# Kernel optimization log

Hardware: AMD Instinct MI355X
Metric: run time of the kernel (lower is better)

## Reference

```python
import jax, jax.numpy as jnp
import numpy as np

N = 50000; E = 800000; B = 500; L = 42
F_IN = 35; HEADS = 10; F_H = 35; F_G = 350
VOCAB = 26; EMB = 128; NF = 16; OUT_DIM = 128; K = 8
NEG_SLOPE = 0.2


def setup_inputs() -> dict:
    key = jax.random.key(0)
    ks = jax.random.split(key, 16)
    inp = {}
    inp['x'] = jax.random.normal(ks[0], (N, F_IN), jnp.float32)
    inp['edge_index'] = jax.random.randint(ks[1], (2, E), 0, N, dtype=jnp.int32)
    inp['batch'] = jnp.sort(jax.random.randint(ks[2], (N,), 0, B, dtype=jnp.int32))
    inp['target'] = jax.random.randint(ks[3], (B, L), 0, VOCAB, dtype=jnp.int32)
    # --- learned parameters ---
    inp['W_gat'] = jax.random.normal(ks[4], (F_IN, HEADS * F_H), jnp.float32) * 0.1
    inp['att_src'] = jax.random.normal(ks[5], (HEADS, F_H), jnp.float32) * 0.1
    inp['att_dst'] = jax.random.normal(ks[6], (HEADS, F_H), jnp.float32) * 0.1
    inp['b_gat'] = jnp.zeros((HEADS * F_H,), jnp.float32)
    inp['W_gcn'] = jax.random.normal(ks[7], (F_G, F_G), jnp.float32) * 0.05
    inp['b_gcn'] = jnp.zeros((F_G,), jnp.float32)
    inp['W_fcg1'] = jax.random.normal(ks[8], (2 * F_G, 1500), jnp.float32) * 0.03
    inp['b_fcg1'] = jnp.zeros((1500,), jnp.float32)
    inp['W_fcg2'] = jax.random.normal(ks[9], (1500, OUT_DIM), jnp.float32) * 0.03
    inp['b_fcg2'] = jnp.zeros((OUT_DIM,), jnp.float32)
    inp['emb_xt'] = jax.random.normal(ks[10], (VOCAB, EMB), jnp.float32) * 0.1
    inp['W_conv'] = jax.random.normal(ks[11], (NF, EMB, K), jnp.float32) * 0.05
    inp['b_conv'] = jnp.zeros((NF,), jnp.float32)
    inp['W_fcxt'] = jax.random.normal(ks[12], (NF * 35, OUT_DIM), jnp.float32) * 0.05
    inp['b_fcxt'] = jnp.zeros((OUT_DIM,), jnp.float32)
    inp['W_fc1'] = jax.random.normal(ks[13], (256, 512), jnp.float32) * 0.05
    inp['b_fc1'] = jnp.zeros((512,), jnp.float32)
    inp['W_out'] = jax.random.normal(ks[14], (512, 1), jnp.float32) * 0.05
    inp['b_out'] = jnp.zeros((1,), jnp.float32)
    return inp


def _add_self_loops(edge_index):
    loop = jnp.arange(N, dtype=edge_index.dtype)
    src = jnp.concatenate([edge_index[0], loop])
    dst = jnp.concatenate([edge_index[1], loop])
    return src, dst


def _gat_conv(x, src, dst, W, att_src, att_dst, b):
    # h: [N, H, C]
    h = (x @ W).reshape(N, HEADS, F_H)
    a_s = jnp.einsum('nhc,hc->nh', h, att_src)  # [N, H]
    a_d = jnp.einsum('nhc,hc->nh', h, att_dst)
    e = jax.nn.leaky_relu(a_s[src] + a_d[dst], NEG_SLOPE)  # [Etot, H]
    # segment softmax over incoming edges per destination node, per head
    m = jax.ops.segment_max(e, dst, num_segments=N)
    m = jnp.where(jnp.isfinite(m), m, 0.0)
    ex = jnp.exp(e - m[dst])
    den = jax.ops.segment_sum(ex, dst, num_segments=N)
    alpha = ex / (den[dst] + 1e-16)  # [Etot, H]
    out = jax.ops.segment_sum(h[src] * alpha[:, :, None], dst, num_segments=N)
    return out.reshape(N, HEADS * F_H) + b, alpha


def _gcn_conv(x, src, dst, W, b):
    deg = jax.ops.segment_sum(jnp.ones_like(dst, jnp.float32), dst, num_segments=N)
    dinv = jnp.where(deg > 0, deg ** -0.5, 0.0)
    norm = dinv[src] * dinv[dst]  # symmetric normalization
    h = x @ W
    return jax.ops.segment_sum(h[src] * norm[:, None], dst, num_segments=N) + b


def reference(x, edge_index, batch, target, W_gat, att_src, att_dst, b_gat,
              W_gcn, b_gcn, W_fcg1, b_fcg1, W_fcg2, b_fcg2, emb_xt,
              W_conv, b_conv, W_fcxt, b_fcxt, W_fc1, b_fc1, W_out, b_out):
    src, dst = _add_self_loops(edge_index)
    # --- graph branch ---
    xg, alpha = _gat_conv(x, src, dst, W_gat, att_src, att_dst, b_gat)
    xg = jax.nn.relu(xg)
    xg = jax.nn.relu(_gcn_conv(xg, src, dst, W_gcn, b_gcn))
    # global max + mean pool per graph
    gmax = jax.ops.segment_max(xg, batch, num_segments=B)
    gsum = jax.ops.segment_sum(xg, batch, num_segments=B)
    cnt = jax.ops.segment_sum(jnp.ones((N,), jnp.float32), batch, num_segments=B)
    gmean = gsum / jnp.maximum(cnt, 1.0)[:, None]
    xg = jnp.concatenate([gmax, gmean], axis=1)  # [B, 700]
    xg = jax.nn.relu(xg @ W_fcg1 + b_fcg1)
    xg = xg @ W_fcg2 + b_fcg2  # [B, 128] (dropout is identity in eval)
    # --- protein branch ---
    emb = emb_xt[target]                      # [B, L, 128]
    emb = jnp.transpose(emb, (0, 2, 1))       # [B, 128, L]
    conv = jax.lax.conv_general_dilated(
        emb, W_conv, window_strides=(1,), padding='VALID',
        dimension_numbers=('NCH', 'OIH', 'NCH'))  # [B, 16, 35]
    conv = conv + b_conv[None, :, None]
    xt = conv.reshape(B, NF * 35)
    xt = xt @ W_fcxt + b_fcxt                 # [B, 128]
    # --- fusion ---
    xc = jnp.concatenate([xg, xt], axis=1)    # [B, 256]
    xc = jax.nn.relu(xc @ W_fc1 + b_fc1)
    out = jax.nn.sigmoid(xc @ W_out + b_out)  # [B, 1]
    return out, alpha
```

## Files before the change

kernel.cpp:

```cpp
#include <hip/hip_runtime.h>
#include <math.h>

#define NN 50000
#define EE 800000
#define BB 500
#define LL 42
#define NHEAD 10
#define FH 35
#define FG 350
#define ETOT (EE + NN)
#define NCHUNK ((NN + 511) / 512)

#define KPAD 384
#define MPAD 50048
#define MB2  512

typedef unsigned short ushort_t;
typedef __attribute__((ext_vector_type(8))) short short8v;
typedef __attribute__((ext_vector_type(4))) float float4v;

__device__ __forceinline__ float lrelu(float x) { return x > 0.f ? x : 0.2f * x; }

__device__ __forceinline__ ushort_t f2bf(float f) {
    unsigned int u = __float_as_uint(f);
    u += 0x7fffu + ((u >> 16) & 1u);
    return (ushort_t)(u >> 16);
}
__device__ __forceinline__ float bflo(unsigned u) { return __uint_as_float(u << 16); }
__device__ __forceinline__ float bfhi(unsigned u) { return __uint_as_float(u & 0xffff0000u); }
__device__ __forceinline__ float bfu(ushort_t u) { return __uint_as_float(((unsigned)u) << 16); }

__device__ __forceinline__ void async_cp16(const void* g, void* l) {
    __builtin_amdgcn_global_load_lds((const __attribute__((address_space(1))) unsigned int*)g,
                                     (__attribute__((address_space(3))) unsigned int*)l, 16, 0, 0);
}

__global__ __launch_bounds__(256) void k_init(int* deg, int* cur) {
    int i = blockIdx.x * 256 + threadIdx.x;
    if (i < NN) { deg[i] = 1; cur[i] = 0; }
}

__global__ __launch_bounds__(256) void k_deg(const int* __restrict__ ei, int* deg) {
    int i = blockIdx.x * 256 + threadIdx.x;
    if (i < EE) atomicAdd(&deg[ei[EE + i]], 1);
}

__global__ __launch_bounds__(512) void k_scan1(const int* __restrict__ deg, int* part) {
    int i = blockIdx.x * 512 + threadIdx.x;
    int lane = threadIdx.x & 63, wv = threadIdx.x >> 6;
    int x = (i < NN) ? deg[i] : 0;
    #pragma unroll
    for (int d = 32; d; d >>= 1) x += __shfl_xor(x, d);
    __shared__ int wsum[8];
    if (lane == 0) wsum[wv] = x;
    __syncthreads();
    if (threadIdx.x == 0) {
        int s = 0;
        #pragma unroll
        for (int w = 0; w < 8; w++) s += wsum[w];
        part[blockIdx.x] = s;
    }
}

__global__ __launch_bounds__(64) void k_scan2(const int* __restrict__ part, int* pscan) {
    int l = threadIdx.x;
    int v0 = (l < NCHUNK) ? part[l] : 0;
    #pragma unroll
    for (int d = 1; d < 64; d <<= 1) { int t = __shfl_up(v0, d); if (l >= d) v0 += t; }
    int tot0 = __shfl(v0, 63);
    int v1 = (64 + l < NCHUNK) ? part[64 + l] : 0;
    #pragma unroll
    for (int d = 1; d < 64; d <<= 1) { int t = __shfl_up(v1, d); if (l >= d) v1 += t; }
    v1 += tot0;
    if (l < NCHUNK) pscan[l] = v0;
    if (64 + l < NCHUNK) pscan[64 + l] = v1;
}

__global__ __launch_bounds__(512) void k_scan3(const int* __restrict__ deg, const int* __restrict__ pscan,
                                               int* offs) {
    int i = blockIdx.x * 512 + threadIdx.x;
    int lane = threadIdx.x & 63, wv = threadIdx.x >> 6;
    int x = (i < NN) ? deg[i] : 0;
    int incl = x;
    #pragma unroll
    for (int d = 1; d < 64; d <<= 1) { int t = __shfl_up(incl, d); if (lane >= d) incl += t; }
    __shared__ int wtot[8];
    if (lane == 63) wtot[wv] = incl;
    __syncthreads();
    int woff = 0;
    for (int w = 0; w < wv; w++) woff += wtot[w];
    int base = (blockIdx.x == 0) ? 0 : pscan[blockIdx.x - 1];
    if (i < NN) offs[i] = base + woff + incl - x;
}

__global__ __launch_bounds__(256) void k_scatter(const int* __restrict__ ei, const int* __restrict__ offs,
                                                 int* cur, int* csr_src) {
    int i = blockIdx.x * 256 + threadIdx.x;
    if (i < EE) {
        int s = ei[i], d = ei[EE + i];
        int slot = atomicAdd(&cur[d], 1);
        csr_src[offs[d] + slot] = s;
    } else if (i < ETOT) {
        int v = i - EE;
        int slot = atomicAdd(&cur[v], 1);
        csr_src[offs[v] + slot] = v;
    }
}

__global__ __launch_bounds__(256) void k_dinv(const int* __restrict__ deg, float* dinv) {
    int i = blockIdx.x * 256 + threadIdx.x;
    if (i < NN) dinv[i] = rsqrtf((float)deg[i]);
}

__global__ __launch_bounds__(256) void k_prep_xf(const float* __restrict__ x, ushort_t* __restrict__ xfb) {
    int i = blockIdx.x * 256 + threadIdx.x;
    if (i >= NN * 40) return;
    int n = i / 40, c = i % 40;
    xfb[i] = (c < 35) ? f2bf(x[n * 35 + c]) : (ushort_t)0;
}

__global__ __launch_bounds__(256) void k_prep_att(const float* __restrict__ W_gat, const float* __restrict__ att_s,
                                                  const float* __restrict__ att_d,
                                                  float* __restrict__ wS, float* __restrict__ wD) {
    int i = blockIdx.x * 256 + threadIdx.x;
    if (i >= FG) return;
    int hd = i / 35, c = i % 35;
    float ss = 0.f, dd = 0.f;
    for (int cc = 0; cc < 35; cc++) {
        float w = W_gat[c * FG + hd * 35 + cc];
        ss += w * att_s[hd * 35 + cc];
        dd += w * att_d[hd * 35 + cc];
    }
    wS[i] = ss;
    wD[i] = dd;
}

__global__ __launch_bounds__(256) void k_prep_wbd(const float* __restrict__ W_gat, ushort_t* __restrict__ Wt) {
    int i = blockIdx.x * 256 + threadIdx.x;
    if (i >= KPAD * KPAD) return;
    int n = i / KPAD, k = i % KPAD;
    float v = 0.f;
    if (n < FG && k < FG && (k / 35) == (n / 35)) v = W_gat[(k % 35) * FG + n];
    Wt[i] = f2bf(v);
}

__global__ __launch_bounds__(256) void k_prep_wgcn(const float* __restrict__ W, ushort_t* __restrict__ Wt) {
    int i = blockIdx.x * 256 + threadIdx.x;
    if (i >= KPAD * KPAD) return;
    int n = i / KPAD, k = i % KPAD;
    float v = (n < FG && k < FG) ? W[k * FG + n] : 0.f;
    Wt[i] = f2bf(v);
}

__global__ __launch_bounds__(256) void k_prep_w(const float* __restrict__ W, ushort_t* __restrict__ Wt,
                                                int K, int N, int KP, int NP) {
    int i = blockIdx.x * 256 + threadIdx.x;
    if (i >= KP * NP) return;
    int k = i / NP, n = i % NP;
    float v = (k < K && n < N) ? W[(size_t)k * N + n] : 0.f;
    Wt[(size_t)n * KP + k] = f2bf(v);
}

__global__ __launch_bounds__(256) void k_cast_pad(const float* __restrict__ src, ushort_t* __restrict__ dst,
                                                  int M, int K, int MP, int KP) {
    int i = blockIdx.x * 256 + threadIdx.x;
    if (i >= MP * KP) return;
    int r = i / KP, k = i % KP;
    dst[i] = (r < M && k < K) ? f2bf(src[(size_t)r * K + k]) : (ushort_t)0;
}

__global__ __launch_bounds__(256) void k_mfma(const ushort_t* __restrict__ A, const ushort_t* __restrict__ Bt,
                                              void* __restrict__ C, int M, int Nv, int ldc, int lda,
                                              int ksteps, const float* __restrict__ bias, int act, int bf16out,
                                              int bdiag) {
    __shared__ ushort_t As[128 * 64];
    __shared__ ushort_t Bs[64 * 64];
    int tid = threadIdx.x;
    int wid = tid >> 6, lane = tid & 63;
    int m0 = blockIdx.y * 128, n0 = blockIdx.x * 64;
    int wm0 = (wid >> 1) * 64, wn0 = (wid & 1) * 32;
    int srow = tid >> 3;
    int scol = (tid & 7) * 8;
    float4v acc[4][2] = {{{0.f,0.f,0.f,0.f},{0.f,0.f,0.f,0.f}},
                         {{0.f,0.f,0.f,0.f},{0.f,0.f,0.f,0.f}},
                         {{0.f,0.f,0.f,0.f},{0.f,0.f,0.f,0.f}},
                         {{0.f,0.f,0.f,0.f},{0.f,0.f,0.f,0.f}}};
    int a_off = (wm0 + (lane & 15)) * 64 + (lane >> 4) * 8;
    int b_off = (wn0 + (lane & 15)) * 64 + (lane >> 4) * 8;
    int ks0 = 0, ks1 = ksteps;
    if (bdiag) {
        int hlo = n0 / 35;
        int hhi = (n0 + 63) / 35; if (hhi > 9) hhi = 9;
        ks0 = (hlo * 35) >> 6;
        ks1 = ((hhi + 1) * 35 + 63) >> 6;
    }
    for (int ks = ks0; ks < ks1; ks++) {
        int k0 = ks * 64;
        #pragma unroll
        for (int r = 0; r < 4; r++) {
            const ushort_t* g = A + (size_t)(m0 + r * 32 + srow) * lda + k0 + scol;
            async_cp16(g, As + (r * 256 + tid) * 8);
        }
        #pragma unroll
        for (int r = 0; r < 2; r++) {
            const ushort_t* g = Bt + (size_t)(n0 + r * 32 + srow) * lda + k0 + scol;
            async_cp16(g, Bs + (r * 256 + tid) * 8);
        }
        __syncthreads();
        #pragma unroll
        for (int kh = 0; kh < 2; kh++) {
            short8v b0 = *(const short8v*)&Bs[b_off + kh * 32];
            short8v b1 = *(const short8v*)&Bs[b_off + 16 * 64 + kh * 32];
            #pragma unroll
            for (int mi = 0; mi < 4; mi++) {
                short8v a = *(const short8v*)&As[a_off + mi * 16 * 64 + kh * 32];
                acc[mi][0] = __builtin_amdgcn_mfma_f32_16x16x32_bf16(a, b0, acc[mi][0], 0, 0, 0);
                acc[mi][1] = __builtin_amdgcn_mfma_f32_16x16x32_bf16(a, b1, acc[mi][1], 0, 0, 0);
            }
        }
        __syncthreads();
    }
    int lm = m0 + wm0 + (lane >> 4) * 4;
    int lc = n0 + wn0 + (lane & 15);
    #pragma unroll
    for (int mi = 0; mi < 4; mi++) {
        #pragma unroll
        for (int ni = 0; ni < 2; ni++) {
            int col = lc + ni * 16;
            float bv = (bias != nullptr && col < Nv) ? bias[col] : 0.f;
            #pragma unroll
            for (int r = 0; r < 4; r++) {
                int row = lm + mi * 16 + r;
                if (row >= M) continue;
                float v = acc[mi][ni][r] + bv;
                if (act) v = fmaxf(v, 0.f);
                if (col >= Nv) v = 0.f;
                if (bf16out) ((ushort_t*)C)[(size_t)row * ldc + col] = f2bf(v);
                else         ((float*)C)[(size_t)row * ldc + col] = v;
            }
        }
    }
}

__global__ __launch_bounds__(256) void k_att2(const float* __restrict__ x, const float* __restrict__ wS,
                                              const float* __restrict__ wD, float* __restrict__ a_s,
                                              float* __restrict__ a_d) {
    int tid = blockIdx.x * 256 + threadIdx.x;
    if (tid >= NN * NHEAD) return;
    int n = tid / NHEAD, hd = tid % NHEAD;
    const float* xr = x + (size_t)n * 35;
    const float* ws = wS + hd * 35;
    const float* wd = wD + hd * 35;
    float as = 0.f, ad = 0.f;
    #pragma unroll
    for (int c = 0; c < 35; c++) { float v = xr[c]; as += v * ws[c]; ad += v * wd[c]; }
    a_s[tid] = as;
    a_d[tid] = ad;
}

__global__ __launch_bounds__(256) void k_gat_agg(const ushort_t* __restrict__ xfb, const float* __restrict__ a_s,
                                                 const float* __restrict__ a_d,
                                                 const int* __restrict__ csr_src,
                                                 const int* __restrict__ offs, const int* __restrict__ deg,
                                                 ushort_t* __restrict__ Zb, float* __restrict__ denArr) {
    int wid = (blockIdx.x * blockDim.x + threadIdx.x) >> 6;
    int lane = threadIdx.x & 63;
    if (wid >= NN) return;
    int o0 = offs[wid], d = deg[wid];
    bool mine = (lane < NHEAD);
    float adv = mine ? a_d[wid * NHEAD + lane] : 0.f;
    int f0 = lane, f1 = lane + 64, f2 = lane + 128, f3 = lane + 192, f4 = lane + 256, f5 = lane + 320;
    int h0 = f0 / 35, h1 = f1 / 35, h2 = f2 / 35, h3 = f3 / 35, h4 = f4 / 35;
    int h5 = (f5 < FG) ? f5 / 35 : 0;
    int c0 = f0 % 35, c1 = f1 % 35, c2 = f2 % 35, c3 = f3 % 35, c4 = f4 % 35;
    int c5 = (f5 < FG) ? f5 % 35 : 0;
    float den = 0.f;
    float ac0 = 0.f, ac1 = 0.f, ac2 = 0.f, ac3 = 0.f, ac4 = 0.f, ac5 = 0.f;
    int i = 0;
    for (; i + 2 <= d; i += 2) {
        int s0 = csr_src[o0 + i], s1 = csr_src[o0 + i + 1];
        const ushort_t* x0 = xfb + (size_t)s0 * 40;
        const ushort_t* x1 = xfb + (size_t)s1 * 40;
        float as0 = mine ? a_s[s0 * NHEAD + lane] : 0.f;
        float as1 = mine ? a_s[s1 * NHEAD + lane] : 0.f;
        ushort_t v00 = x0[c0], v01 = x0[c1], v02 = x0[c2], v03 = x0[c3], v04 = x0[c4], v05 = x0[c5];
        ushort_t v10 = x1[c0], v11 = x1[c1], v12 = x1[c2], v13 = x1[c3], v14 = x1[c4], v15 = x1[c5];
        float ex0 = __expf(lrelu(as0 + adv));
        float ex1 = __expf(lrelu(as1 + adv));
        den += ex0 + ex1;
        ac0 += __shfl(ex0, h0) * bfu(v00) + __shfl(ex1, h0) * bfu(v10);
        ac1 += __shfl(ex0, h1) * bfu(v01) + __shfl(ex1, h1) * bfu(v11);
        ac2 += __shfl(ex0, h2) * bfu(v02) + __shfl(ex1, h2) * bfu(v12);
        ac3 += __shfl(ex0, h3) * bfu(v03) + __shfl(ex1, h3) * bfu(v13);
        ac4 += __shfl(ex0, h4) * bfu(v04) + __shfl(ex1, h4) * bfu(v14);
        ac5 += __shfl(ex0, h5) * bfu(v05) + __shfl(ex1, h5) * bfu(v15);
    }
    for (; i < d; i++) {
        int s = csr_src[o0 + i];
        const ushort_t* xr = xfb + (size_t)s * 40;
        float asv = mine ? a_s[s * NHEAD + lane] : 0.f;
        float ex = __expf(lrelu(asv + adv));
        den += ex;
        ac0 += __shfl(ex, h0) * bfu(xr[c0]);
        ac1 += __shfl(ex, h1) * bfu(xr[c1]);
        ac2 += __shfl(ex, h2) * bfu(xr[c2]);
        ac3 += __shfl(ex, h3) * bfu(xr[c3]);
        ac4 += __shfl(ex, h4) * bfu(xr[c4]);
        ac5 += __shfl(ex, h5) * bfu(xr[c5]);
    }
    float rden = 1.f / (den + 1e-16f);
    if (mine) denArr[wid * NHEAD + lane] = den;
    ushort_t* zr = Zb + (size_t)wid * KPAD;
    __builtin_nontemporal_store(f2bf(ac0 * __shfl(rden, h0)), &zr[f0]);
    __builtin_nontemporal_store(f2bf(ac1 * __shfl(rden, h1)), &zr[f1]);
    __builtin_nontemporal_store(f2bf(ac2 * __shfl(rden, h2)), &zr[f2]);
    __builtin_nontemporal_store(f2bf(ac3 * __shfl(rden, h3)), &zr[f3]);
    __builtin_nontemporal_store(f2bf(ac4 * __shfl(rden, h4)), &zr[f4]);
    __builtin_nontemporal_store((f5 < FG) ? f2bf(ac5 * __shfl(rden, h5)) : (ushort_t)0, &zr[f5]);
}

__global__ __launch_bounds__(256) void k_alpha(const int* __restrict__ ei, const float* __restrict__ a_s,
                                               const float* __restrict__ a_d, const float* __restrict__ den,
                                               float* __restrict__ alphaOut) {
    int i = blockIdx.x * 256 + threadIdx.x;
    if (i >= ETOT * NHEAD) return;
    int e = i / NHEAD, hd = i % NHEAD;
    int s, dst;
    if (e < EE) { s = ei[e]; dst = ei[EE + e]; }
    else { s = dst = e - EE; }
    float ex = __expf(lrelu(a_s[s * NHEAD + hd] + a_d[dst * NHEAD + hd]));
    __builtin_nontemporal_store(ex / (den[dst * NHEAD + hd] + 1e-16f), &alphaOut[i]);
}

__global__ __launch_bounds__(256) void k_gcn_agg(const ushort_t* __restrict__ h2b,
                                                 const int* __restrict__ csr_src,
                                                 const int* __restrict__ offs, const int* __restrict__ deg,
                                                 const float* __restrict__ dinv, const float* __restrict__ b_gcn,
                                                 float* __restrict__ xg2) {
    int wid = (blockIdx.x * blockDim.x + threadIdx.x) >> 6;
    int lane = threadIdx.x & 63;
    if (wid >= NN) return;
    int o0 = offs[wid], d = deg[wid];
    float wv = dinv[wid];
    float aL0 = 0.f, aH0 = 0.f, aL1 = 0.f, aH1 = 0.f, aL2 = 0.f, aH2 = 0.f;
    const unsigned* h32 = (const unsigned*)h2b;
    int i = 0;
    for (; i + 2 <= d; i += 2) {
        int s0 = csr_src[o0 + i], s1 = csr_src[o0 + i + 1];
        float w0 = dinv[s0], w1 = dinv[s1];
        const unsigned* h0 = h32 + (size_t)s0 * (KPAD / 2);
        const unsigned* h1 = h32 + (size_t)s1 * (KPAD / 2);
        unsigned u00 = h0[lane], u01 = h0[lane + 64], u02 = h0[lane + 128];
        unsigned u10 = h1[lane], u11 = h1[lane + 64], u12 = h1[lane + 128];
        aL0 += w0 * bflo(u00) + w1 * bflo(u10);
        aH0 += w0 * bfhi(u00) + w1 * bfhi(u10);
        aL1 += w0 * bflo(u01) + w1 * bflo(u11);
        aH1 += w0 * bfhi(u01) + w1 * bfhi(u11);
        aL2 += w0 * bflo(u02) + w1 * bflo(u12);
        aH2 += w0 * bfhi(u02) + w1 * bfhi(u12);
    }
    for (; i < d; i++) {
        int s = csr_src[o0 + i];
        float ws = dinv[s];
        const unsigned* hr = h32 + (size_t)s * (KPAD / 2);
        unsigned u0 = hr[lane], u1 = hr[lane + 64], u2 = hr[lane + 128];
        aL0 += ws * bflo(u0);  aH0 += ws * bfhi(u0);
        aL1 += ws * bflo(u1);  aH1 += ws * bfhi(u1);
        aL2 += ws * bflo(u2);  aH2 += ws * bfhi(u2);
    }
    float* orow = xg2 + (size_t)wid * FG;
    {
        int f = 2 * lane;
        __builtin_nontemporal_store(fmaxf(wv * aL0 + b_gcn[f], 0.f), &orow[f]);
        __builtin_nontemporal_store(fmaxf(wv * aH0 + b_gcn[f + 1], 0.f), &orow[f + 1]);
    }
    {
        int f = 128 + 2 * lane;
        __builtin_nontemporal_store(fmaxf(wv * aL1 + b_gcn[f], 0.f), &orow[f]);
        __builtin_nontemporal_store(fmaxf(wv * aH1 + b_gcn[f + 1], 0.f), &orow[f + 1]);
    }
    {
        int f = 256 + 2 * lane;
        if (f < FG) {
            __builtin_nontemporal_store(fmaxf(wv * aL2 + b_gcn[f], 0.f), &orow[f]);
            __builtin_nontemporal_store(fmaxf(wv * aH2 + b_gcn[f + 1], 0.f), &orow[f + 1]);
        }
    }
}

__device__ __forceinline__ int lowerB(const int* a, int n, int key) {
    int lo = 0, hi = n;
    while (lo < hi) { int mid = (lo + hi) >> 1; if (a[mid] < key) lo = mid + 1; else hi = mid; }
    return lo;
}

__global__ __launch_bounds__(384) void k_pool(const float* __restrict__ xg2, const int* __restrict__ batch,
                                              float* __restrict__ pooled) {
    int g = blockIdx.x;
    int f = threadIdx.x;
    int s = lowerB(batch, NN, g);
    int e = lowerB(batch, NN, g + 1);
    if (f >= FG) return;
    float mx = -INFINITY, sm = 0.f;
    int n = s;
    for (; n + 4 <= e; n += 4) {
        float v0 = xg2[(size_t)(n + 0) * FG + f];
        float v1 = xg2[(size_t)(n + 1) * FG + f];
        float v2 = xg2[(size_t)(n + 2) * FG + f];
        float v3 = xg2[(size_t)(n + 3) * FG + f];
        mx = fmaxf(fmaxf(mx, v0), fmaxf(fmaxf(v1, v2), v3));
        sm += v0 + v1 + v2 + v3;
    }
    for (; n < e; n++) {
        float v = xg2[(size_t)n * FG + f];
        mx = fmaxf(mx, v);
        sm += v;
    }
    int cnt = e - s;
    pooled[g * 700 + f] = mx;
    pooled[g * 700 + FG + f] = sm / fmaxf((float)cnt, 1.f);
}

__global__ __launch_bounds__(256) void k_conv(const int* __restrict__ target, const float* __restrict__ emb,
                                              const float* __restrict__ Wc, const float* __restrict__ bc,
                                              float* __restrict__ xt) {
    __shared__ float embL[26 * 132];
    __shared__ float WL[16 * 8 * 128];
    __shared__ int   tgL[2 * LL];
    int tid = threadIdx.x;
    int b0 = blockIdx.x * 2;
    for (int i = tid; i < 26 * 128; i += 256) {
        int r = i >> 7, e = i & 127;
        embL[r * 132 + e] = emb[i];
    }
    for (int i = tid; i < 16384; i += 256) {
        int f = i >> 10, rem = i & 1023, k = rem >> 7, e = rem & 127;
        WL[i] = Wc[f * 1024 + e * 8 + k];
    }
    if (tid < 2 * LL) tgL[tid] = target[b0 * LL + tid];
    __syncthreads();
    #pragma unroll
    for (int pass = 0; pass < 2; pass++) {
        int r = tid + pass * 256;
        if (r >= 280) break;
        int bl = r / 140, rem = r % 140;
        int fq = rem / 35, t = rem % 35;
        const int* tg = &tgL[bl * LL];
        float ac0 = 0.f, ac1 = 0.f, ac2 = 0.f, ac3 = 0.f;
        for (int k = 0; k < 8; k++) {
            const float* er = &embL[tg[t + k] * 132];
            const float* w0 = &WL[((fq * 4 + 0) * 8 + k) * 128];
            const float* w1 = &WL[((fq * 4 + 1) * 8 + k) * 128];
            const float* w2 = &WL[((fq * 4 + 2) * 8 + k) * 128];
            const float* w3 = &WL[((fq * 4 + 3) * 8 + k) * 128];
            #pragma unroll 8
            for (int e = 0; e < 128; e += 4) {
                float4 a = *(const float4*)&er[e];
                float4 q0 = *(const float4*)&w0[e];
                float4 q1 = *(const float4*)&w1[e];
                float4 q2 = *(const float4*)&w2[e];
                float4 q3 = *(const float4*)&w3[e];
                ac0 += a.x * q0.x + a.y * q0.y + a.z * q0.z + a.w * q0.w;
                ac1 += a.x * q1.x + a.y * q1.y + a.z * q1.z + a.w * q1.w;
                ac2 += a.x * q2.x + a.y * q2.y + a.z * q2.z + a.w * q2.w;
                ac3 += a.x * q3.x + a.y * q3.y + a.z * q3.z + a.w * q3.w;
            }
        }
        int b = b0 + bl, fb = fq * 4;
        xt[b * 560 + (fb + 0) * 35 + t] = ac0 + bc[fb + 0];
        xt[b * 560 + (fb + 1) * 35 + t] = ac1 + bc[fb + 1];
        xt[b * 560 + (fb + 2) * 35 + t] = ac2 + bc[fb + 2];
        xt[b * 560 + (fb + 3) * 35 + t] = ac3 + bc[fb + 3];
    }
}

__global__ __launch_bounds__(256) void k_out(const float* __restrict__ f1, const float* __restrict__ W_out,
                                             const float* __restrict__ b_out, float* __restrict__ out) {
    int wid = (blockIdx.x * blockDim.x + threadIdx.x) >> 6;
    int lane = threadIdx.x & 63;
    if (wid >= BB) return;
    const float* xr = f1 + (size_t)wid * 512;
    float acc = 0.f;
    #pragma unroll
    for (int k = 0; k < 8; k++) acc += xr[lane + k * 64] * W_out[lane + k * 64];
    #pragma unroll
    for (int d = 32; d; d >>= 1) acc += __shfl_xor(acc, d);
    if (lane == 0) out[wid] = 1.f / (1.f + __expf(-(acc + b_out[0])));
}

extern "C" void kernel_launch(void* const* d_in, const int* in_sizes, int n_in,
                              void* d_out, int out_size, void* d_ws, size_t ws_size,
                              hipStream_t stream) {
    const float* x      = (const float*)d_in[0];
    const int*   ei     = (const int*)d_in[1];
    const int*   batch  = (const int*)d_in[2];
    const int*   target = (const int*)d_in[3];
    const float* W_gat  = (const float*)d_in[4];
    const float* att_s  = (const float*)d_in[5];
    const float* att_d  = (const float*)d_in[6];
    const float* b_gat  = (const float*)d_in[7];
    const float* W_gcn  = (const float*)d_in[8];
    const float* b_gcn  = (const float*)d_in[9];
    const float* W_fcg1 = (const float*)d_in[10];
    const float* b_fcg1 = (const float*)d_in[11];
    const float* W_fcg2 = (const float*)d_in[12];
    const float* b_fcg2 = (const float*)d_in[13];
    const float* embxt  = (const float*)d_in[14];
    const float* W_conv = (const float*)d_in[15];
    const float* b_conv = (const float*)d_in[16];
    const float* W_fcxt = (const float*)d_in[17];
    const float* b_fcxt = (const float*)d_in[18];
    const float* W_fc1  = (const float*)d_in[19];
    const float* b_fc1  = (const float*)d_in[20];
    const float* W_out  = (const float*)d_in[21];
    const float* b_out  = (const float*)d_in[22];

    float* out_sig  = (float*)d_out;
    float* alphaOut = (float*)d_out + BB;

    size_t o = 0;
    auto alloc = [&](size_t bytes) -> void* {
        o = (o + 255) & ~(size_t)255;
        void* p = (char*)d_ws + o;
        o += bytes;
        return p;
    };
    int*   deg     = (int*)alloc((size_t)NN * 4);
    int*   cur     = (int*)alloc((size_t)NN * 4);
    int*   offs    = (int*)alloc((size_t)NN * 4);
    int*   part    = (int*)alloc(128 * 4);
    int*   pscan   = (int*)alloc(128 * 4);
    int*   csr_src = (int*)alloc((size_t)ETOT * 4);
    float* dinv    = (float*)alloc((size_t)NN * 4);
    float* a_s     = (float*)alloc((size_t)NN * NHEAD * 4);
    float* a_d     = (float*)alloc((size_t)NN * NHEAD * 4);
    float* denArr  = (float*)alloc((size_t)NN * NHEAD * 4);
    ushort_t* xfb  = (ushort_t*)alloc((size_t)NN * 40 * 2);
    float* wS      = (float*)alloc((size_t)FG * 4);
    float* wD      = (float*)alloc((size_t)FG * 4);
    ushort_t* WtBD = (ushort_t*)alloc((size_t)KPAD * KPAD * 2);
    ushort_t* WtGC = (ushort_t*)alloc((size_t)KPAD * KPAD * 2);
    ushort_t* WtF1 = (ushort_t*)alloc((size_t)1536 * 704 * 2);
    ushort_t* WtF2 = (ushort_t*)alloc((size_t)128 * 1536 * 2);
    ushort_t* WtFX = (ushort_t*)alloc((size_t)128 * 576 * 2);
    ushort_t* WtFC = (ushort_t*)alloc((size_t)512 * 256 * 2);
    float* pooled  = (float*)alloc((size_t)BB * 700 * 4);
    ushort_t* pooledb = (ushort_t*)alloc((size_t)MB2 * 704 * 2);
    ushort_t* t1b  = (ushort_t*)alloc((size_t)MB2 * 1536 * 2);
    float* xt      = (float*)alloc((size_t)BB * 560 * 4);
    ushort_t* xtb  = (ushort_t*)alloc((size_t)MB2 * 576 * 2);
    ushort_t* xcb  = (ushort_t*)alloc((size_t)MB2 * 256 * 2);
    float* f1      = (float*)alloc((size_t)MB2 * 512 * 4);
    ushort_t* hb   = (ushort_t*)alloc((size_t)MPAD * KPAD * 2);
    char*  R2      = (char*)alloc((size_t)NN * FG * 4);
    ushort_t* xg1b = (ushort_t*)R2;
    float* xg2     = (float*)R2;
    (void)ws_size; (void)n_in; (void)in_sizes; (void)out_size;

    auto mfma = [&](const ushort_t* A, const ushort_t* Bt, void* C, const float* bias,
                    int M2, int Nv, int NP, int ldc, int KP, int act, int bf16out, int bdiag) {
        dim3 g(NP / 64, M2 / 128);
        k_mfma<<<g, 256, 0, stream>>>(A, Bt, C, M2, Nv, ldc, KP, KP / 64, bias, act, bf16out, bdiag);
    };

    k_init<<<(NN + 255) / 256, 256, 0, stream>>>(deg, cur);
    k_deg<<<(EE + 255) / 256, 256, 0, stream>>>(ei, deg);
    k_scan1<<<NCHUNK, 512, 0, stream>>>(deg, part);
    k_scan2<<<1, 64, 0, stream>>>(part, pscan);
    k_scan3<<<NCHUNK, 512, 0, stream>>>(deg, pscan, offs);
    k_scatter<<<(ETOT + 255) / 256, 256, 0, stream>>>(ei, offs, cur, csr_src);
    k_dinv<<<(NN + 255) / 256, 256, 0, stream>>>(deg, dinv);

    k_prep_xf<<<(NN * 40 + 255) / 256, 256, 0, stream>>>(x, xfb);
    k_prep_att<<<2, 256, 0, stream>>>(W_gat, att_s, att_d, wS, wD);
    k_prep_wbd<<<(KPAD * KPAD + 255) / 256, 256, 0, stream>>>(W_gat, WtBD);
    k_prep_wgcn<<<(KPAD * KPAD + 255) / 256, 256, 0, stream>>>(W_gcn, WtGC);
    k_prep_w<<<(704 * 1536 + 255) / 256, 256, 0, stream>>>(W_fcg1, WtF1, 700, 1500, 704, 1536);
    k_prep_w<<<(1536 * 128 + 255) / 256, 256, 0, stream>>>(W_fcg2, WtF2, 1500, 128, 1536, 128);
    k_prep_w<<<(576 * 128 + 255) / 256, 256, 0, stream>>>(W_fcxt, WtFX, 560, 128, 576, 128);
    k_prep_w<<<(256 * 512 + 255) / 256, 256, 0, stream>>>(W_fc1, WtFC, 256, 512, 256, 512);

    k_att2<<<(NN * NHEAD + 255) / 256, 256, 0, stream>>>(x, wS, wD, a_s, a_d);
    k_gat_agg<<<(NN + 3) / 4, 256, 0, stream>>>(xfb, a_s, a_d, csr_src, offs, deg, hb, denArr);
    k_alpha<<<(ETOT * NHEAD + 255) / 256, 256, 0, stream>>>(ei, a_s, a_d, denArr, alphaOut);
    mfma(hb, WtBD, xg1b, b_gat, MPAD, FG, KPAD, KPAD, KPAD, 1, 1, 1);

    mfma(xg1b, WtGC, hb, nullptr, MPAD, KPAD, KPAD, KPAD, KPAD, 0, 1, 0);
    k_gcn_agg<<<(NN + 3) / 4, 256, 0, stream>>>(hb, csr_src, offs, deg, dinv, b_gcn, xg2);

    k_pool<<<BB, 384, 0, stream>>>(xg2, batch, pooled);
    k_cast_pad<<<(MB2 * 704 + 255) / 256, 256, 0, stream>>>(pooled, pooledb, BB, 700, MB2, 704);
    mfma(pooledb, WtF1, t1b, b_fcg1, MB2, 1500, 1536, 1536, 704, 1, 1, 0);
    mfma(t1b, WtF2, xcb, b_fcg2, MB2, 128, 128, 256, 1536, 0, 1, 0);
    k_conv<<<250, 256, 0, stream>>>(target, embxt, W_conv, b_conv, xt);
    k_cast_pad<<<(MB2 * 576 + 255) / 256, 256, 0, stream>>>(xt, xtb, BB, 560, MB2, 576);
    mfma(xtb, WtFX, xcb + 128, b_fcxt, MB2, 128, 128, 256, 576, 0, 1, 0);
    mfma(xcb, WtFC, f1, b_fc1, MB2, 512, 512, 512, 256, 1, 0, 0);
    k_out<<<(BB + 3) / 4, 256, 0, stream>>>(f1, W_out, b_out, out_sig);
}
```

Baseline: 637.3 us.

## Repack GAT aggregation output per head to 36 and narrow GCN hidden stride

The GAT aggregation now lays out each head in 36 columns (35 plus one pad), so each lane handles packed bf16 pairs with 32-bit loads and stores instead of six scalar ushort gathers. The block-diagonal weight and its k-range limits are updated to match the 36-wide head layout. The GCN transform now writes its bf16 output with a 352-column stride instead of 384, which cuts the bytes gathered per neighbour in the GCN aggregation. Because the padded rows beyond N are no longer written, a tail-zero kernel clears them, and the new column limit (nst) skips stores past the narrower stride.

```diff
diff --git a/kernel.cpp b/kernel.cpp
--- a/kernel.cpp
+++ b/kernel.cpp
@@ -12,6 +12,7 @@
 #define NCHUNK ((NN + 511) / 512)
 
 #define KPAD 384
+#define LDH2 352
 #define MPAD 50048
 #define MB2  512
 
@@ -28,7 +29,9 @@
 }
 __device__ __forceinline__ float bflo(unsigned u) { return __uint_as_float(u << 16); }
 __device__ __forceinline__ float bfhi(unsigned u) { return __uint_as_float(u & 0xffff0000u); }
-__device__ __forceinline__ float bfu(ushort_t u) { return __uint_as_float(((unsigned)u) << 16); }
+__device__ __forceinline__ unsigned packbf(float a, float b) {
+    return (unsigned)f2bf(a) | ((unsigned)f2bf(b) << 16);
+}
 
 __device__ __forceinline__ void async_cp16(const void* g, void* l) {
     __builtin_amdgcn_global_load_lds((const __attribute__((address_space(1))) unsigned int*)g,
@@ -139,8 +142,9 @@
     int i = blockIdx.x * 256 + threadIdx.x;
     if (i >= KPAD * KPAD) return;
     int n = i / KPAD, k = i % KPAD;
+    int hd = k / 36, cc = k % 36;
     float v = 0.f;
-    if (n < FG && k < FG && (k / 35) == (n / 35)) v = W_gat[(k % 35) * FG + n];
+    if (n < FG && cc < 35 && hd == n / 35) v = W_gat[cc * FG + n];
     Wt[i] = f2bf(v);
 }
 
@@ -169,10 +173,16 @@
     dst[i] = (r < M && k < K) ? f2bf(src[(size_t)r * K + k]) : (ushort_t)0;
 }
 
+__global__ __launch_bounds__(256) void k_zero_tail(ushort_t* buf) {
+    int i = blockIdx.x * 256 + threadIdx.x;
+    int total = (MPAD - NN) * KPAD;
+    if (i < total) buf[(size_t)NN * KPAD + i] = 0;
+}
+
 __global__ __launch_bounds__(256) void k_mfma(const ushort_t* __restrict__ A, const ushort_t* __restrict__ Bt,
                                               void* __restrict__ C, int M, int Nv, int ldc, int lda,
                                               int ksteps, const float* __restrict__ bias, int act, int bf16out,
-                                              int bdiag) {
+                                              int bdiag, int nst) {
     __shared__ ushort_t As[128 * 64];
     __shared__ ushort_t Bs[64 * 64];
     int tid = threadIdx.x;
@@ -191,8 +201,8 @@
     if (bdiag) {
         int hlo = n0 / 35;
         int hhi = (n0 + 63) / 35; if (hhi > 9) hhi = 9;
-        ks0 = (hlo * 35) >> 6;
-        ks1 = ((hhi + 1) * 35 + 63) >> 6;
+        ks0 = (hlo * 36) >> 6;
+        ks1 = (hhi * 36 + 36 + 63) >> 6;
     }
     for (int ks = ks0; ks < ks1; ks++) {
         int k0 = ks * 64;
@@ -227,6 +237,7 @@
         #pragma unroll
         for (int ni = 0; ni < 2; ni++) {
             int col = lc + ni * 16;
+            if (col >= nst) continue;
             float bv = (bias != nullptr && col < Nv) ? bias[col] : 0.f;
             #pragma unroll
             for (int r = 0; r < 4; r++) {
@@ -269,54 +280,54 @@
     int o0 = offs[wid], d = deg[wid];
     bool mine = (lane < NHEAD);
     float adv = mine ? a_d[wid * NHEAD + lane] : 0.f;
-    int f0 = lane, f1 = lane + 64, f2 = lane + 128, f3 = lane + 192, f4 = lane + 256, f5 = lane + 320;
-    int h0 = f0 / 35, h1 = f1 / 35, h2 = f2 / 35, h3 = f3 / 35, h4 = f4 / 35;
-    int h5 = (f5 < FG) ? f5 / 35 : 0;
-    int c0 = f0 % 35, c1 = f1 % 35, c2 = f2 % 35, c3 = f3 % 35, c4 = f4 % 35;
-    int c5 = (f5 < FG) ? f5 % 35 : 0;
+    int h1 = lane / 18,          c1 = lane % 18;
+    int h2 = (lane + 64) / 18,   c2 = (lane + 64) % 18;
+    bool g3 = lane < 52;
+    int h3 = g3 ? (lane + 128) / 18 : 0;
+    int c3 = g3 ? (lane + 128) % 18 : 0;
     float den = 0.f;
-    float ac0 = 0.f, ac1 = 0.f, ac2 = 0.f, ac3 = 0.f, ac4 = 0.f, ac5 = 0.f;
+    float a1l = 0.f, a1h = 0.f, a2l = 0.f, a2h = 0.f, a3l = 0.f, a3h = 0.f;
+    const unsigned* x32 = (const unsigned*)xfb;
     int i = 0;
     for (; i + 2 <= d; i += 2) {
         int s0 = csr_src[o0 + i], s1 = csr_src[o0 + i + 1];
-        const ushort_t* x0 = xfb + (size_t)s0 * 40;
-        const ushort_t* x1 = xfb + (size_t)s1 * 40;
+        const unsigned* x0 = x32 + (size_t)s0 * 20;
+        const unsigned* x1 = x32 + (size_t)s1 * 20;
         float as0 = mine ? a_s[s0 * NHEAD + lane] : 0.f;
         float as1 = mine ? a_s[s1 * NHEAD + lane] : 0.f;
-        ushort_t v00 = x0[c0], v01 = x0[c1], v02 = x0[c2], v03 = x0[c3], v04 = x0[c4], v05 = x0[c5];
-        ushort_t v10 = x1[c0], v11 = x1[c1], v12 = x1[c2], v13 = x1[c3], v14 = x1[c4], v15 = x1[c5];
+        unsigned u01 = x0[c1], u02 = x0[c2], u03 = x0[c3];
+        unsigned u11 = x1[c1], u12 = x1[c2], u13 = x1[c3];
         float ex0 = __expf(lrelu(as0 + adv));
         float ex1 = __expf(lrelu(as1 + adv));
         den += ex0 + ex1;
-        ac0 += __shfl(ex0, h0) * bfu(v00) + __shfl(ex1, h0) * bfu(v10);
-        ac1 += __shfl(ex0, h1) * bfu(v01) + __shfl(ex1, h1) * bfu(v11);
-        ac2 += __shfl(ex0, h2) * bfu(v02) + __shfl(ex1, h2) * bfu(v12);
-        ac3 += __shfl(ex0, h3) * bfu(v03) + __shfl(ex1, h3) * bfu(v13);
-        ac4 += __shfl(ex0, h4) * bfu(v04) + __shfl(ex1, h4) * bfu(v14);
-        ac5 += __shfl(ex0, h5) * bfu(v05) + __shfl(ex1, h5) * bfu(v15);
+        float e01 = __shfl(ex0, h1), e02 = __shfl(ex0, h2), e03 = __shfl(ex0, h3);
+        float e11 = __shfl(ex1, h1), e12 = __shfl(ex1, h2), e13 = __shfl(ex1, h3);
+        a1l += e01 * bflo(u01) + e11 * bflo(u11);
+        a1h += e01 * bfhi(u01) + e11 * bfhi(u11);
+        a2l += e02 * bflo(u02) + e12 * bflo(u12);
+        a2h += e02 * bfhi(u02) + e12 * bfhi(u12);
+        a3l += e03 * bflo(u03) + e13 * bflo(u13);
+        a3h += e03 * bfhi(u03) + e13 * bfhi(u13);
     }
     for (; i < d; i++) {
         int s = csr_src[o0 + i];
-        const ushort_t* xr = xfb + (size_t)s * 40;
-        float asv = mine ? a_s[s * NHEAD + lane] : 0.f;
-        float ex = __expf(lrelu(asv + adv));
-        den += ex;
-        ac0 += __shfl(ex, h0) * bfu(xr[c0]);
-        ac1 += __shfl(ex, h1) * bfu(xr[c1]);
-        ac2 += __shfl(ex, h2) * bfu(xr[c2]);
-        ac3 += __shfl(ex, h3) * bfu(xr[c3]);
-        ac4 += __shfl(ex, h4) * bfu(xr[c4]);
-        ac5 += __shfl(ex, h5) * bfu(xr[c5]);
+        const unsigned* x0 = x32 + (size_t)s * 20;
+        float as0 = mine ? a_s[s * NHEAD + lane] : 0.f;
+        unsigned u01 = x0[c1], u02 = x0[c2], u03 = x0[c3];
+        float ex0 = __expf(lrelu(as0 + adv));
+        den += ex0;
+        float e01 = __shfl(ex0, h1), e02 = __shfl(ex0, h2), e03 = __shfl(ex0, h3);
+        a1l += e01 * bflo(u01);  a1h += e01 * bfhi(u01);
+        a2l += e02 * bflo(u02);  a2h += e02 * bfhi(u02);
+        a3l += e03 * bflo(u03);  a3h += e03 * bfhi(u03);
     }
     float rden = 1.f / (den + 1e-16f);
     if (mine) denArr[wid * NHEAD + lane] = den;
-    ushort_t* zr = Zb + (size_t)wid * KPAD;
-    __builtin_nontemporal_store(f2bf(ac0 * __shfl(rden, h0)), &zr[f0]);
-    __builtin_nontemporal_store(f2bf(ac1 * __shfl(rden, h1)), &zr[f1]);
-    __builtin_nontemporal_store(f2bf(ac2 * __shfl(rden, h2)), &zr[f2]);
-    __builtin_nontemporal_store(f2bf(ac3 * __shfl(rden, h3)), &zr[f3]);
-    __builtin_nontemporal_store(f2bf(ac4 * __shfl(rden, h4)), &zr[f4]);
-    __builtin_nontemporal_store((f5 < FG) ? f2bf(ac5 * __shfl(rden, h5)) : (ushort_t)0, &zr[f5]);
+    float r1 = __shfl(rden, h1), r2 = __shfl(rden, h2), r3 = __shfl(rden, h3);
+    unsigned* zr = (unsigned*)(Zb + (size_t)wid * KPAD);
+    __builtin_nontemporal_store(packbf(a1l * r1, a1h * r1), &zr[lane]);
+    __builtin_nontemporal_store(packbf(a2l * r2, a2h * r2), &zr[lane + 64]);
+    __builtin_nontemporal_store(g3 ? packbf(a3l * r3, a3h * r3) : 0u, &zr[lane + 128]);
 }
 
 __global__ __launch_bounds__(256) void k_alpha(const int* __restrict__ ei, const float* __restrict__ a_s,
@@ -342,16 +353,18 @@
     if (wid >= NN) return;
     int o0 = offs[wid], d = deg[wid];
     float wv = dinv[wid];
+    bool g3 = lane < 48;
+    int w3 = g3 ? (lane + 128) : 0;
     float aL0 = 0.f, aH0 = 0.f, aL1 = 0.f, aH1 = 0.f, aL2 = 0.f, aH2 = 0.f;
     const unsigned* h32 = (const unsigned*)h2b;
     int i = 0;
     for (; i + 2 <= d; i += 2) {
         int s0 = csr_src[o0 + i], s1 = csr_src[o0 + i + 1];
         float w0 = dinv[s0], w1 = dinv[s1];
-        const unsigned* h0 = h32 + (size_t)s0 * (KPAD / 2);
-        const unsigned* h1 = h32 + (size_t)s1 * (KPAD / 2);
-        unsigned u00 = h0[lane], u01 = h0[lane + 64], u02 = h0[lane + 128];
-        unsigned u10 = h1[lane], u11 = h1[lane + 64], u12 = h1[lane + 128];
+        const unsigned* h0 = h32 + (size_t)s0 * (LDH2 / 2);
+        const unsigned* h1 = h32 + (size_t)s1 * (LDH2 / 2);
+        unsigned u00 = h0[lane], u01 = h0[lane + 64], u02 = h0[w3];
+        unsigned u10 = h1[lane], u11 = h1[lane + 64], u12 = h1[w3];
         aL0 += w0 * bflo(u00) + w1 * bflo(u10);
         aH0 += w0 * bfhi(u00) + w1 * bfhi(u10);
         aL1 += w0 * bflo(u01) + w1 * bflo(u11);
@@ -362,8 +375,8 @@
     for (; i < d; i++) {
         int s = csr_src[o0 + i];
         float ws = dinv[s];
-        const unsigned* hr = h32 + (size_t)s * (KPAD / 2);
-        unsigned u0 = hr[lane], u1 = hr[lane + 64], u2 = hr[lane + 128];
+        const unsigned* hr = h32 + (size_t)s * (LDH2 / 2);
+        unsigned u0 = hr[lane], u1 = hr[lane + 64], u2 = hr[w3];
         aL0 += ws * bflo(u0);  aH0 += ws * bfhi(u0);
         aL1 += ws * bflo(u1);  aH1 += ws * bfhi(u1);
         aL2 += ws * bflo(u2);  aH2 += ws * bfhi(u2);
@@ -558,9 +571,9 @@
     (void)ws_size; (void)n_in; (void)in_sizes; (void)out_size;
 
     auto mfma = [&](const ushort_t* A, const ushort_t* Bt, void* C, const float* bias,
-                    int M2, int Nv, int NP, int ldc, int KP, int act, int bf16out, int bdiag) {
+                    int M2, int Nv, int NP, int ldc, int KP, int act, int bf16out, int bdiag, int nst) {
         dim3 g(NP / 64, M2 / 128);
-        k_mfma<<<g, 256, 0, stream>>>(A, Bt, C, M2, Nv, ldc, KP, KP / 64, bias, act, bf16out, bdiag);
+        k_mfma<<<g, 256, 0, stream>>>(A, Bt, C, M2, Nv, ldc, KP, KP / 64, bias, act, bf16out, bdiag, nst);
     };
 
     k_init<<<(NN + 255) / 256, 256, 0, stream>>>(deg, cur);
@@ -579,22 +592,23 @@
     k_prep_w<<<(1536 * 128 + 255) / 256, 256, 0, stream>>>(W_fcg2, WtF2, 1500, 128, 1536, 128);
     k_prep_w<<<(576 * 128 + 255) / 256, 256, 0, stream>>>(W_fcxt, WtFX, 560, 128, 576, 128);
     k_prep_w<<<(256 * 512 + 255) / 256, 256, 0, stream>>>(W_fc1, WtFC, 256, 512, 256, 512);
+    k_zero_tail<<<((MPAD - NN) * KPAD + 255) / 256, 256, 0, stream>>>(hb);
 
     k_att2<<<(NN * NHEAD + 255) / 256, 256, 0, stream>>>(x, wS, wD, a_s, a_d);
     k_gat_agg<<<(NN + 3) / 4, 256, 0, stream>>>(xfb, a_s, a_d, csr_src, offs, deg, hb, denArr);
     k_alpha<<<(ETOT * NHEAD + 255) / 256, 256, 0, stream>>>(ei, a_s, a_d, denArr, alphaOut);
-    mfma(hb, WtBD, xg1b, b_gat, MPAD, FG, KPAD, KPAD, KPAD, 1, 1, 1);
-
-    mfma(xg1b, WtGC, hb, nullptr, MPAD, KPAD, KPAD, KPAD, KPAD, 0, 1, 0);
+    mfma(hb, WtBD, xg1b, b_gat, MPAD, FG, KPAD, KPAD, KPAD, 1, 1, 1, KPAD);
+
+    mfma(xg1b, WtGC, hb, nullptr, MPAD, FG, KPAD, LDH2, KPAD, 0, 1, 0, LDH2);
     k_gcn_agg<<<(NN + 3) / 4, 256, 0, stream>>>(hb, csr_src, offs, deg, dinv, b_gcn, xg2);
 
     k_pool<<<BB, 384, 0, stream>>>(xg2, batch, pooled);
     k_cast_pad<<<(MB2 * 704 + 255) / 256, 256, 0, stream>>>(pooled, pooledb, BB, 700, MB2, 704);
-    mfma(pooledb, WtF1, t1b, b_fcg1, MB2, 1500, 1536, 1536, 704, 1, 1, 0);
-    mfma(t1b, WtF2, xcb, b_fcg2, MB2, 128, 128, 256, 1536, 0, 1, 0);
+    mfma(pooledb, WtF1, t1b, b_fcg1, MB2, 1500, 1536, 1536, 704, 1, 1, 0, 1536);
+    mfma(t1b, WtF2, xcb, b_fcg2, MB2, 128, 128, 256, 1536, 0, 1, 0, 128);
     k_conv<<<250, 256, 0, stream>>>(target, embxt, W_conv, b_conv, xt);
     k_cast_pad<<<(MB2 * 576 + 255) / 256, 256, 0, stream>>>(xt, xtb, BB, 560, MB2, 576);
-    mfma(xtb, WtFX, xcb + 128, b_fcxt, MB2, 128, 128, 256, 576, 0, 1, 0);
-    mfma(xcb, WtFC, f1, b_fc1, MB2, 512, 512, 512, 256, 1, 0, 0);
+    mfma(xtb, WtFX, xcb + 128, b_fcxt, MB2, 128, 128, 256, 576, 0, 1, 0, 128);
+    mfma(xcb, WtFC, f1, b_fc1, MB2, 512, 512, 512, 256, 1, 0, 0, 512);
     k_out<<<(BB + 3) / 4, 256, 0, stream>>>(f1, W_out, b_out, out_sig);
 }
```

Result: faster. 605.0 us (-5.1%).
